# Optimization experiments

Measured on AMD Instinct MI355X. Metric: run time of the kernel, lower is better.

## Reference

```python
import jax, jax.numpy as jnp
import numpy as np

N, E, EV, D = 50000, 300000, 100000, 256
BN_EPS = 1e-5


def batchnorm(h, gamma, beta):
    # training-mode BN with batch statistics (biased var, matching torch normalization)
    mu = h.mean(axis=0)
    var = h.var(axis=0)
    return gamma * (h - mu) * jax.lax.rsqrt(var + BN_EPS) + beta


def mlp(h, W1, b1, g1, bt1, W2, b2):
    # Linear -> BN -> ReLU -> (Dropout=identity in eval) -> Linear
    h = h @ W1 + b1
    h = jax.nn.relu(batchnorm(h, g1, bt1))
    return h @ W2 + b2


def gine_conv(x, ei, ea, eps, W1, b1, g1, bt1, W2, b2):
    # message: ReLU(x_src + edge_attr); aggregate: scatter-add at dst; update: MLP((1+eps)*x + aggr)
    m = jax.nn.relu(x[ei[0]] + ea)                       # [E, D]
    aggr = jax.ops.segment_sum(m, ei[1], num_segments=N)  # [N, D]
    return mlp((1.0 + eps) * x + aggr, W1, b1, g1, bt1, W2, b2)


def setup_inputs() -> dict:
    key = jax.random.key(0)
    ks = jax.random.split(key, 16)
    s = 1.0 / np.sqrt(D)
    inp = {
        "x": jax.random.normal(ks[0], (N, D), jnp.float32),
        "edge_index": jax.random.randint(ks[1], (2, E), 0, N, jnp.int64),
        "edge_attr_emb": jax.random.normal(ks[2], (E, D), jnp.float32),
        "v_idx": jax.random.randint(ks[3], (2, EV), 0, N, jnp.int64),
        "v_edge_emb": jax.random.normal(ks[4], (EV, D), jnp.float32),
        # conv_down params
        "eps_down": jnp.zeros((), jnp.float32),
        "W1d": jax.random.normal(ks[5], (D, D), jnp.float32) * s,
        "b1d": jnp.zeros((D,), jnp.float32),
        "g1d": jnp.ones((D,), jnp.float32),
        "bt1d": jnp.zeros((D,), jnp.float32),
        "W2d": jax.random.normal(ks[6], (D, D), jnp.float32) * s,
        "b2d": jnp.zeros((D,), jnp.float32),
        # conv_up params
        "eps_up": jnp.zeros((), jnp.float32),
        "W1u": jax.random.normal(ks[7], (D, D), jnp.float32) * s,
        "b1u": jnp.zeros((D,), jnp.float32),
        "g1u": jnp.ones((D,), jnp.float32),
        "bt1u": jnp.zeros((D,), jnp.float32),
        "W2u": jax.random.normal(ks[8], (D, D), jnp.float32) * s,
        "b2u": jnp.zeros((D,), jnp.float32),
        # final BN + residual scales
        "bn_g": jnp.ones((D,), jnp.float32),
        "bn_b": jnp.zeros((D,), jnp.float32),
        "alpha1": jnp.asarray(1.0, jnp.float32),
        "alpha2": jnp.asarray(0.01, jnp.float32),
    }
    return inp


def reference(x, edge_index, edge_attr_emb, v_idx, v_edge_emb,
              eps_down, W1d, b1d, g1d, bt1d, W2d, b2d,
              eps_up, W1u, b1u, g1u, bt1u, W2u, b2u,
              bn_g, bn_b, alpha1, alpha2):
    h_down = gine_conv(x, edge_index, edge_attr_emb, eps_down, W1d, b1d, g1d, bt1d, W2d, b2d)
    h_up = gine_conv(x, v_idx, v_edge_emb, eps_up, W1u, b1u, g1u, bt1u, W2u, b2u)
    out = x + alpha1 * h_down + alpha2 * h_up
    return jax.nn.relu(batchnorm(out, bn_g, bn_b))
```

## Files before the change

### kernel.cpp

```cpp
#include <hip/hip_runtime.h>
#include <math.h>

#define N_NODES 50000
#define DIM 256
#define NE 300000
#define NEV 100000
#define BM 64
#define BK 64
#define NSLOT 8
#define GRID_PER ((N_NODES + BM - 1) / BM)

typedef float f32x4 __attribute__((ext_vector_type(4)));
typedef short s16x8 __attribute__((ext_vector_type(8)));

__device__ inline unsigned short f2bf(float f) {
    unsigned u = __float_as_uint(f);
    u += 0x7FFF + ((u >> 16) & 1);
    return (unsigned short)(u >> 16);
}
__device__ inline float bf2f(unsigned short s) {
    return __uint_as_float(((unsigned)s) << 16);
}
__device__ inline int swz(int row, int kg) {
    return row * BK + ((kg ^ (row & 7)) << 3);
}

__global__ __launch_bounds__(256) void prepw_kernel(
    const float* __restrict__ W1d, const float* __restrict__ W2d,
    const float* __restrict__ W1u, const float* __restrict__ W2u,
    unsigned short* __restrict__ Wt)
{
    int b = blockIdx.x;
    int w = b >> 8, n = b & 255, k = threadIdx.x;
    const float* W = (w == 0) ? W1d : (w == 1) ? W2d : (w == 2) ? W1u : W2u;
    Wt[(size_t)w * DIM * DIM + (size_t)n * DIM + k] = f2bf(W[(size_t)k * DIM + n]);
}

__global__ __launch_bounds__(256) void hist2_kernel(
    const int* __restrict__ ei, const int* __restrict__ vi,
    int* __restrict__ degD, int* __restrict__ degU)
{
    int i = blockIdx.x * blockDim.x + threadIdx.x;
    if (i < NE) atomicAdd(&degD[ei[NE + i]], 1);
    else if (i < NE + NEV) { int j = i - NE; atomicAdd(&degU[vi[NEV + j]], 1); }
}

__global__ __launch_bounds__(1024) void scan2_kernel(
    int* __restrict__ offD, int* __restrict__ curD,
    int* __restrict__ offU, int* __restrict__ curU)
{
    int* deg_offsets = (blockIdx.x == 0) ? offD : offU;
    int* cursor      = (blockIdx.x == 0) ? curD : curU;
    int E            = (blockIdx.x == 0) ? NE : NEV;
    __shared__ int part[1024];
    int t = threadIdx.x;
    const int CH = (N_NODES + 1023) / 1024;
    int beg = t * CH;
    int end = min(beg + CH, N_NODES);
    int s = 0;
    for (int i = beg; i < end; i++) s += deg_offsets[i];
    part[t] = s;
    __syncthreads();
    for (int off = 1; off < 1024; off <<= 1) {
        int v = part[t];
        int u = (t >= off) ? part[t - off] : 0;
        __syncthreads();
        part[t] = v + u;
        __syncthreads();
    }
    int run = (t > 0) ? part[t - 1] : 0;
    for (int i = beg; i < end; i++) {
        int dv = deg_offsets[i];
        deg_offsets[i] = run;
        cursor[i] = run;
        run += dv;
    }
    if (t == 1023) deg_offsets[N_NODES] = E;
}

__global__ __launch_bounds__(256) void fill2_kernel(
    const int* __restrict__ ei, const int* __restrict__ vi,
    int* __restrict__ curD, int* __restrict__ curU,
    int2* __restrict__ pairsD, int2* __restrict__ pairsU)
{
    int i = blockIdx.x * blockDim.x + threadIdx.x;
    if (i < NE) {
        int s = ei[i], d = ei[NE + i];
        int pos = atomicAdd(&curD[d], 1);
        pairsD[pos] = make_int2(i, s);
    } else if (i < NE + NEV) {
        int j = i - NE;
        int s = vi[j], d = vi[NEV + j];
        int pos = atomicAdd(&curU[d], 1);
        pairsU[pos] = make_int2(j, s);
    }
}

__device__ inline f32x4 ld4(const float* p) { return *(const f32x4*)p; }
__device__ inline f32x4 ldnt4(const float* p) {
    return __builtin_nontemporal_load((const f32x4*)p);
}
__device__ inline void acc_relu(f32x4& acc, f32x4 a, f32x4 b) {
    acc.x += fmaxf(a.x + b.x, 0.f);
    acc.y += fmaxf(a.y + b.y, 0.f);
    acc.z += fmaxf(a.z + b.z, 0.f);
    acc.w += fmaxf(a.w + b.w, 0.f);
}

__global__ __launch_bounds__(256) void gather2_kernel(
    const float* __restrict__ x, const float* __restrict__ ea,
    const float* __restrict__ vea,
    const int* __restrict__ offD, const int2* __restrict__ pairsD,
    const int* __restrict__ offU, const int2* __restrict__ pairsU,
    const float* __restrict__ epsd, const float* __restrict__ epsu,
    unsigned short* __restrict__ hD, unsigned short* __restrict__ hU)
{
    __shared__ f32x4 part[2][64];
    int warp = threadIdx.x >> 6;
    int lane = threadIdx.x & 63;
    int slotn = warp >> 1;
    int half = warp & 1;
    int nidx = blockIdx.x * 2 + slotn;
    bool down = nidx < N_NODES;
    int node = down ? nidx : nidx - N_NODES;
    const int* off      = down ? offD   : offU;
    const int2* pairs   = down ? pairsD : pairsU;
    const float* eat    = down ? ea     : vea;
    unsigned short* h   = down ? hD     : hU;
    float epsv = 1.0f + (down ? epsd[0] : epsu[0]);

    int beg = off[node], end = off[node + 1];
    f32x4 acc = {0.f, 0.f, 0.f, 0.f};
    int cofs = lane * 4;
    int p = beg + half;
    for (; p + 2 < end; p += 4) {
        int2 q0 = pairs[p], q1 = pairs[p + 2];
        f32x4 a0 = ld4(x + (size_t)q0.y * DIM + cofs);
        f32x4 b0 = ldnt4(eat + (size_t)q0.x * DIM + cofs);
        f32x4 a1 = ld4(x + (size_t)q1.y * DIM + cofs);
        f32x4 b1 = ldnt4(eat + (size_t)q1.x * DIM + cofs);
        acc_relu(acc, a0, b0);
        acc_relu(acc, a1, b1);
    }
    if (p < end) {
        int2 q0 = pairs[p];
        f32x4 a0 = ld4(x + (size_t)q0.y * DIM + cofs);
        f32x4 b0 = ldnt4(eat + (size_t)q0.x * DIM + cofs);
        acc_relu(acc, a0, b0);
    }
    if (half == 1) part[slotn][lane] = acc;
    __syncthreads();
    if (half == 0) {
        f32x4 o = part[slotn][lane];
        acc.x += o.x; acc.y += o.y; acc.z += o.z; acc.w += o.w;
        f32x4 xv = ld4(x + (size_t)node * DIM + cofs);
        acc.x = fmaf(epsv, xv.x, acc.x);
        acc.y = fmaf(epsv, xv.y, acc.y);
        acc.z = fmaf(epsv, xv.z, acc.z);
        acc.w = fmaf(epsv, xv.w, acc.w);
        ushort4 pk;
        pk.x = f2bf(acc.x); pk.y = f2bf(acc.y);
        pk.z = f2bf(acc.z); pk.w = f2bf(acc.w);
        *(ushort4*)(h + (size_t)node * DIM + cofs) = pk;
    }
}

__global__ __launch_bounds__(256) void scatter_kernel(
    const float* __restrict__ x, const float* __restrict__ ea,
    const int* __restrict__ idx, int E, float* __restrict__ buf)
{
    int wid = blockIdx.x * (blockDim.x >> 6) + (threadIdx.x >> 6);
    int lane = threadIdx.x & 63;
    if (wid >= E) return;
    int s = idx[wid];
    int d = idx[E + wid];
    float4 a = ((const float4*)(x + (size_t)s * DIM))[lane];
    float4 b = ((const float4*)(ea + (size_t)wid * DIM))[lane];
    float* dst = buf + (size_t)d * DIM + lane * 4;
    atomicAdd(dst + 0, fmaxf(a.x + b.x, 0.f));
    atomicAdd(dst + 1, fmaxf(a.y + b.y, 0.f));
    atomicAdd(dst + 2, fmaxf(a.z + b.z, 0.f));
    atomicAdd(dst + 3, fmaxf(a.w + b.w, 0.f));
}

__global__ __launch_bounds__(256) void conv_kernel(
    const float* __restrict__ x, const float* __restrict__ aggr,
    const float* __restrict__ eps_p, unsigned short* __restrict__ h)
{
    float epsv = 1.0f + eps_p[0];
    int i = blockIdx.x * blockDim.x + threadIdx.x;
    const int total = N_NODES * (DIM / 4);
    for (int f = i; f < total; f += gridDim.x * blockDim.x) {
        float4 xv = ((const float4*)x)[f];
        float4 av = ((const float4*)aggr)[f];
        ushort4 pk;
        pk.x = f2bf(fmaf(epsv, xv.x, av.x));
        pk.y = f2bf(fmaf(epsv, xv.y, av.y));
        pk.z = f2bf(fmaf(epsv, xv.z, av.z));
        pk.w = f2bf(fmaf(epsv, xv.w, av.w));
        ((ushort4*)h)[f] = pk;
    }
}

__global__ __launch_bounds__(256) void gemm1_both(
    const unsigned short* __restrict__ hD, const unsigned short* __restrict__ hU,
    const unsigned short* __restrict__ Wt1d, const unsigned short* __restrict__ Wt1u,
    const float* __restrict__ b1d, const float* __restrict__ b1u,
    unsigned short* __restrict__ t1D, unsigned short* __restrict__ t1U,
    float* __restrict__ sumD, float* __restrict__ sqD,
    float* __restrict__ sumU, float* __restrict__ sqU)
{
    __shared__ unsigned short As[BM * BK];
    __shared__ unsigned short Bs[DIM * BK];
    int blk = blockIdx.x;
    bool down = blk < GRID_PER;
    int bb = down ? blk : blk - GRID_PER;
    const unsigned short* h  = down ? hD   : hU;
    const unsigned short* Wt = down ? Wt1d : Wt1u;
    const float* bias        = down ? b1d  : b1u;
    unsigned short* t1       = down ? t1D  : t1U;
    float* ssum              = down ? sumD : sumU;
    float* ssq               = down ? sqD  : sqU;

    int t = threadIdx.x;
    int w = t >> 6, l = t & 63, lrow = l & 15, kgrp = l >> 4;
    int row0 = bb * BM;

    f32x4 acc[16];
    #pragma unroll
    for (int i = 0; i < 16; ++i) acc[i] = (f32x4){0.f, 0.f, 0.f, 0.f};

    for (int k0 = 0; k0 < DIM; k0 += BK) {
        __syncthreads();
        #pragma unroll
        for (int it = 0; it < 2; ++it) {
            int g = it * 256 + t, row = g >> 3, kg = g & 7;
            int gr = row0 + row;
            s16x8 v = {0, 0, 0, 0, 0, 0, 0, 0};
            if (gr < N_NODES)
                v = *(const s16x8*)&h[(size_t)gr * DIM + k0 + kg * 8];
            *(s16x8*)&As[swz(row, kg)] = v;
        }
        #pragma unroll
        for (int it = 0; it < 8; ++it) {
            int g = it * 256 + t, row = g >> 3, kg = g & 7;
            s16x8 v = *(const s16x8*)&Wt[(size_t)row * DIM + k0 + kg * 8];
            *(s16x8*)&Bs[swz(row, kg)] = v;
        }
        __syncthreads();
        #pragma unroll
        for (int kk = 0; kk < 2; ++kk) {
            s16x8 af[4], bf[4];
            #pragma unroll
            for (int mi = 0; mi < 4; ++mi)
                af[mi] = *(const s16x8*)&As[swz(mi * 16 + lrow, kk * 4 + kgrp)];
            #pragma unroll
            for (int ni = 0; ni < 4; ++ni)
                bf[ni] = *(const s16x8*)&Bs[swz(w * 64 + ni * 16 + lrow, kk * 4 + kgrp)];
            #pragma unroll
            for (int mi = 0; mi < 4; ++mi)
                #pragma unroll
                for (int ni = 0; ni < 4; ++ni)
                    acc[mi * 4 + ni] = __builtin_amdgcn_mfma_f32_16x16x32_bf16(
                        af[mi], bf[ni], acc[mi * 4 + ni], 0, 0, 0);
        }
    }
    int slot = bb & (NSLOT - 1);
    #pragma unroll
    for (int ni = 0; ni < 4; ++ni) {
        int col = w * 64 + ni * 16 + lrow;
        float bv = bias[col];
        float s = 0.f, q = 0.f;
        #pragma unroll
        for (int mi = 0; mi < 4; ++mi) {
            #pragma unroll
            for (int r = 0; r < 4; ++r) {
                int grow = row0 + mi * 16 + kgrp * 4 + r;
                if (grow < N_NODES) {
                    float v = acc[mi * 4 + ni][r] + bv;
                    t1[(size_t)grow * DIM + col] = f2bf(v);
                    s += v; q += v * v;
                }
            }
        }
        s += __shfl_xor(s, 16); q += __shfl_xor(q, 16);
        s += __shfl_xor(s, 32); q += __shfl_xor(q, 32);
        if (kgrp == 0) {
            atomicAdd(&ssum[slot * DIM + col], s);
            atomicAdd(&ssq[slot * DIM + col], q);
        }
    }
}

__device__ inline void bn_finalize(
    const float* ssum, const float* ssq, const float* g, const float* b,
    float* scale, float* shift, int c)
{
    float s = 0.f, q = 0.f;
    #pragma unroll
    for (int k = 0; k < NSLOT; ++k) { s += ssum[k * DIM + c]; q += ssq[k * DIM + c]; }
    const float invN = 1.0f / (float)N_NODES;
    float mu = s * invN;
    float var = q * invN - mu * mu;
    float sc = g[c] * rsqrtf(var + 1e-5f);
    scale[c] = sc;
    shift[c] = b[c] - mu * sc;
}

__global__ __launch_bounds__(256) void gemm2_fused(
    const unsigned short* __restrict__ t1D, const unsigned short* __restrict__ t1U,
    const float* __restrict__ sumD, const float* __restrict__ sqD,
    const float* __restrict__ g1d, const float* __restrict__ bt1d,
    const float* __restrict__ sumU, const float* __restrict__ sqU,
    const float* __restrict__ g1u, const float* __restrict__ bt1u,
    const unsigned short* __restrict__ Wt2d, const unsigned short* __restrict__ Wt2u,
    const float* __restrict__ b2d, const float* __restrict__ b2u,
    const float* __restrict__ a1, const float* __restrict__ a2,
    const float* __restrict__ x, float* __restrict__ out,
    float* __restrict__ sumF, float* __restrict__ sqF)
{
    __shared__ unsigned short As[BM * BK];
    __shared__ unsigned short Bs[DIM * BK];
    __shared__ float scDl[DIM], shDl[DIM], scUl[DIM], shUl[DIM];
    int t = threadIdx.x;
    int w = t >> 6, l = t & 63, lrow = l & 15, kgrp = l >> 4;
    int bb = blockIdx.x;
    int row0 = bb * BM;

    bn_finalize(sumD, sqD, g1d, bt1d, scDl, shDl, t);
    bn_finalize(sumU, sqU, g1u, bt1u, scUl, shUl, t);
    float a1v = a1[0], a2v = a2[0];

    f32x4 acc[16], accO[16];
    #pragma unroll
    for (int i = 0; i < 16; ++i) acc[i] = (f32x4){0.f, 0.f, 0.f, 0.f};

    for (int k0 = 0; k0 < DIM; k0 += BK) {
        __syncthreads();
        #pragma unroll
        for (int it = 0; it < 2; ++it) {
            int g = it * 256 + t, row = g >> 3, kg = g & 7;
            int gr = row0 + row;
            s16x8 pack = {0, 0, 0, 0, 0, 0, 0, 0};
            if (gr < N_NODES) {
                s16x8 tv = *(const s16x8*)(t1D + (size_t)gr * DIM + k0 + kg * 8);
                #pragma unroll
                for (int j = 0; j < 8; ++j) {
                    int c = k0 + kg * 8 + j;
                    pack[j] = f2bf(fmaxf(fmaf(bf2f((unsigned short)tv[j]), scDl[c], shDl[c]), 0.f));
                }
            }
            *(s16x8*)&As[swz(row, kg)] = pack;
        }
        #pragma unroll
        for (int it = 0; it < 8; ++it) {
            int g = it * 256 + t, row = g >> 3, kg = g & 7;
            s16x8 v = *(const s16x8*)&Wt2d[(size_t)row * DIM + k0 + kg * 8];
            *(s16x8*)&Bs[swz(row, kg)] = v;
        }
        __syncthreads();
        #pragma unroll
        for (int kk = 0; kk < 2; ++kk) {
            s16x8 af[4], bf[4];
            #pragma unroll
            for (int mi = 0; mi < 4; ++mi)
                af[mi] = *(const s16x8*)&As[swz(mi * 16 + lrow, kk * 4 + kgrp)];
            #pragma unroll
            for (int ni = 0; ni < 4; ++ni)
                bf[ni] = *(const s16x8*)&Bs[swz(w * 64 + ni * 16 + lrow, kk * 4 + kgrp)];
            #pragma unroll
            for (int mi = 0; mi < 4; ++mi)
                #pragma unroll
                for (int ni = 0; ni < 4; ++ni)
                    acc[mi * 4 + ni] = __builtin_amdgcn_mfma_f32_16x16x32_bf16(
                        af[mi], bf[ni], acc[mi * 4 + ni], 0, 0, 0);
        }
    }
    #pragma unroll
    for (int ni = 0; ni < 4; ++ni) {
        float bv = b2d[w * 64 + ni * 16 + lrow];
        #pragma unroll
        for (int mi = 0; mi < 4; ++mi) {
            #pragma unroll
            for (int r = 0; r < 4; ++r)
                accO[mi * 4 + ni][r] = a1v * (acc[mi * 4 + ni][r] + bv);
            acc[mi * 4 + ni] = (f32x4){0.f, 0.f, 0.f, 0.f};
        }
    }

    for (int k0 = 0; k0 < DIM; k0 += BK) {
        __syncthreads();
        #pragma unroll
        for (int it = 0; it < 2; ++it) {
            int g = it * 256 + t, row = g >> 3, kg = g & 7;
            int gr = row0 + row;
            s16x8 pack = {0, 0, 0, 0, 0, 0, 0, 0};
            if (gr < N_NODES) {
                s16x8 tv = *(const s16x8*)(t1U + (size_t)gr * DIM + k0 + kg * 8);
                #pragma unroll
                for (int j = 0; j < 8; ++j) {
                    int c = k0 + kg * 8 + j;
                    pack[j] = f2bf(fmaxf(fmaf(bf2f((unsigned short)tv[j]), scUl[c], shUl[c]), 0.f));
                }
            }
            *(s16x8*)&As[swz(row, kg)] = pack;
        }
        #pragma unroll
        for (int it = 0; it < 8; ++it) {
            int g = it * 256 + t, row = g >> 3, kg = g & 7;
            s16x8 v = *(const s16x8*)&Wt2u[(size_t)row * DIM + k0 + kg * 8];
            *(s16x8*)&Bs[swz(row, kg)] = v;
        }
        __syncthreads();
        #pragma unroll
        for (int kk = 0; kk < 2; ++kk) {
            s16x8 af[4], bf[4];
            #pragma unroll
            for (int mi = 0; mi < 4; ++mi)
                af[mi] = *(const s16x8*)&As[swz(mi * 16 + lrow, kk * 4 + kgrp)];
            #pragma unroll
            for (int ni = 0; ni < 4; ++ni)
                bf[ni] = *(const s16x8*)&Bs[swz(w * 64 + ni * 16 + lrow, kk * 4 + kgrp)];
            #pragma unroll
            for (int mi = 0; mi < 4; ++mi)
                #pragma unroll
                for (int ni = 0; ni < 4; ++ni)
                    acc[mi * 4 + ni] = __builtin_amdgcn_mfma_f32_16x16x32_bf16(
                        af[mi], bf[ni], acc[mi * 4 + ni], 0, 0, 0);
        }
    }

    int slot = bb & (NSLOT - 1);
    #pragma unroll
    for (int ni = 0; ni < 4; ++ni) {
        int col = w * 64 + ni * 16 + lrow;
        float bvU = b2u[col];
        float s = 0.f, q = 0.f;
        #pragma unroll
        for (int mi = 0; mi < 4; ++mi) {
            #pragma unroll
            for (int r = 0; r < 4; ++r) {
                int grow = row0 + mi * 16 + kgrp * 4 + r;
                if (grow < N_NODES) {
                    size_t o = (size_t)grow * DIM + col;
                    float v = x[o] + accO[mi * 4 + ni][r]
                            + a2v * (acc[mi * 4 + ni][r] + bvU);
                    out[o] = v;
                    s += v; q += v * v;
                }
            }
        }
        s += __shfl_xor(s, 16); q += __shfl_xor(q, 16);
        s += __shfl_xor(s, 32); q += __shfl_xor(q, 32);
        if (kgrp == 0) {
            atomicAdd(&sumF[slot * DIM + col], s);
            atomicAdd(&sqF[slot * DIM + col], q);
        }
    }
}

__global__ __launch_bounds__(256) void bnrelu_kernel(
    float* __restrict__ out,
    const float* __restrict__ sumF, const float* __restrict__ sqF,
    const float* __restrict__ bng, const float* __restrict__ bnb)
{
    __shared__ float scl[DIM], shl[DIM];
    bn_finalize(sumF, sqF, bng, bnb, scl, shl, threadIdx.x);
    __syncthreads();
    int idx = blockIdx.x * blockDim.x + threadIdx.x;
    const int total = N_NODES * (DIM / 4);
    for (int f = idx; f < total; f += gridDim.x * blockDim.x) {
        float4 v = ((float4*)out)[f];
        int c = (f * 4) & (DIM - 1);
        float4 sc = *(const float4*)(scl + c);
        float4 sh = *(const float4*)(shl + c);
        v.x = fmaxf(v.x * sc.x + sh.x, 0.0f);
        v.y = fmaxf(v.y * sc.y + sh.y, 0.0f);
        v.z = fmaxf(v.z * sc.z + sh.z, 0.0f);
        v.w = fmaxf(v.w * sc.w + sh.w, 0.0f);
        ((float4*)out)[f] = v;
    }
}

extern "C" void kernel_launch(void* const* d_in, const int* in_sizes, int n_in,
                              void* d_out, int out_size, void* d_ws, size_t ws_size,
                              hipStream_t stream)
{
    const float* x    = (const float*)d_in[0];
    const int*   ei   = (const int*)  d_in[1];
    const float* ea   = (const float*)d_in[2];
    const int*   vi   = (const int*)  d_in[3];
    const float* vea  = (const float*)d_in[4];
    const float* epsd = (const float*)d_in[5];
    const float* W1d  = (const float*)d_in[6];
    const float* b1d  = (const float*)d_in[7];
    const float* g1d  = (const float*)d_in[8];
    const float* bt1d = (const float*)d_in[9];
    const float* W2d  = (const float*)d_in[10];
    const float* b2d  = (const float*)d_in[11];
    const float* epsu = (const float*)d_in[12];
    const float* W1u  = (const float*)d_in[13];
    const float* b1u  = (const float*)d_in[14];
    const float* g1u  = (const float*)d_in[15];
    const float* bt1u = (const float*)d_in[16];
    const float* W2u  = (const float*)d_in[17];
    const float* b2u  = (const float*)d_in[18];
    const float* bng  = (const float*)d_in[19];
    const float* bnb  = (const float*)d_in[20];
    const float* a1   = (const float*)d_in[21];
    const float* a2   = (const float*)d_in[22];

    float* out = (float*)d_out;

    char* p = (char*)d_ws;
    unsigned short* hD  = (unsigned short*)p;  p += (size_t)N_NODES * DIM * 2;
    unsigned short* hU  = (unsigned short*)p;  p += (size_t)N_NODES * DIM * 2;
    unsigned short* t1D = (unsigned short*)p;  p += (size_t)N_NODES * DIM * 2;
    unsigned short* t1U = (unsigned short*)p;  p += (size_t)N_NODES * DIM * 2;
    unsigned short* Wt  = (unsigned short*)p;  p += (size_t)4 * DIM * DIM * 2;
    char* zero_base = p;
    float* stats = (float*)p;                  p += (size_t)6 * NSLOT * DIM * 4;
    int* offD = (int*)p;                       p += (size_t)(N_NODES + 1) * 4;
    int* offU = (int*)p;                       p += (size_t)(N_NODES + 1) * 4;
    size_t zero_bytes = (size_t)(p - zero_base);
    int* curD = (int*)p;                       p += (size_t)N_NODES * 4;
    int* curU = (int*)p;                       p += (size_t)N_NODES * 4;
    char* union_base = p;
    int2* pairsD = (int2*)p;                   p += (size_t)NE * 8;
    int2* pairsU = (int2*)p;                   p += (size_t)NEV * 8;
    size_t need_csr = (size_t)(p - (char*)d_ws);
    float* aggr = (float*)union_base;
    size_t need_fb = (size_t)(union_base - (char*)d_ws) + (size_t)N_NODES * DIM * 4;
    bool use_csr = ws_size >= need_csr;

    float* sumD = stats;
    float* sqD  = stats + 1 * NSLOT * DIM;
    float* sumU = stats + 2 * NSLOT * DIM;
    float* sqU  = stats + 3 * NSLOT * DIM;
    float* sumF = stats + 4 * NSLOT * DIM;
    float* sqF  = stats + 5 * NSLOT * DIM;

    unsigned short* Wt1d = Wt;
    unsigned short* Wt2d = Wt + 1 * (size_t)DIM * DIM;
    unsigned short* Wt1u = Wt + 2 * (size_t)DIM * DIM;
    unsigned short* Wt2u = Wt + 3 * (size_t)DIM * DIM;

    hipMemsetAsync(zero_base, 0, zero_bytes, stream);
    prepw_kernel<<<4 * DIM, 256, 0, stream>>>(W1d, W2d, W1u, W2u, Wt);

    if (use_csr) {
        hist2_kernel<<<(NE + NEV + 255) / 256, 256, 0, stream>>>(ei, vi, offD, offU);
        scan2_kernel<<<2, 1024, 0, stream>>>(offD, curD, offU, curU);
        fill2_kernel<<<(NE + NEV + 255) / 256, 256, 0, stream>>>(
            ei, vi, curD, curU, pairsD, pairsU);
        gather2_kernel<<<N_NODES, 256, 0, stream>>>(
            x, ea, vea, offD, pairsD, offU, pairsU, epsd, epsu, hD, hU);
    } else if (ws_size >= need_fb) {
        hipMemsetAsync(aggr, 0, (size_t)N_NODES * DIM * 4, stream);
        scatter_kernel<<<(NE + 3) / 4, 256, 0, stream>>>(x, ea, ei, NE, aggr);
        conv_kernel<<<2048, 256, 0, stream>>>(x, aggr, epsd, hD);
        hipMemsetAsync(aggr, 0, (size_t)N_NODES * DIM * 4, stream);
        scatter_kernel<<<(NEV + 3) / 4, 256, 0, stream>>>(x, vea, vi, NEV, aggr);
        conv_kernel<<<2048, 256, 0, stream>>>(x, aggr, epsu, hU);
    }

    gemm1_both<<<2 * GRID_PER, 256, 0, stream>>>(
        hD, hU, Wt1d, Wt1u, b1d, b1u, t1D, t1U, sumD, sqD, sumU, sqU);

    gemm2_fused<<<GRID_PER, 256, 0, stream>>>(
        t1D, t1U, sumD, sqD, g1d, bt1d, sumU, sqU, g1u, bt1u,
        Wt2d, Wt2u, b2d, b2u, a1, a2, x, out, sumF, sqF);

    bnrelu_kernel<<<2048, 256, 0, stream>>>(out, sumF, sqF, bng, bnb);
}
```

Before: 438.4 us.

## Gather from bf16 x copy, pre-swizzle operands, use global_load_lds in GEMMs

Result: faster. 415.1 us (-5.3%).

```diff
diff --git a/kernel.cpp b/kernel.cpp
--- a/kernel.cpp
+++ b/kernel.cpp
@@ -9,6 +9,9 @@
 #define BK 64
 #define NSLOT 8
 #define GRID_PER ((N_NODES + BM - 1) / BM)
+#define PREP_W_BLOCKS (4 * DIM)
+#define PREP_X_BLOCKS 1024
+#define HIST_BLOCKS ((NE + NEV + 255) / 256)
 
 typedef float f32x4 __attribute__((ext_vector_type(4)));
 typedef short s16x8 __attribute__((ext_vector_type(8)));
@@ -24,25 +27,51 @@
 __device__ inline int swz(int row, int kg) {
     return row * BK + ((kg ^ (row & 7)) << 3);
 }
-
-__global__ __launch_bounds__(256) void prepw_kernel(
+__device__ inline void gl16(const unsigned short* g, unsigned short* l) {
+    __builtin_amdgcn_global_load_lds(
+        (const __attribute__((address_space(1))) void*)g,
+        (__attribute__((address_space(3))) void*)l, 16, 0, 0);
+}
+__device__ inline int hdst(int node, int lane) {
+    return ((lane >> 4) << 6) + (((((lane >> 1) & 7)) ^ (node & 7)) << 3)
+         + ((lane & 1) << 2);
+}
+
+__global__ __launch_bounds__(256) void prep_kernel(
     const float* __restrict__ W1d, const float* __restrict__ W2d,
     const float* __restrict__ W1u, const float* __restrict__ W2u,
-    unsigned short* __restrict__ Wt)
-{
-    int b = blockIdx.x;
-    int w = b >> 8, n = b & 255, k = threadIdx.x;
-    const float* W = (w == 0) ? W1d : (w == 1) ? W2d : (w == 2) ? W1u : W2u;
-    Wt[(size_t)w * DIM * DIM + (size_t)n * DIM + k] = f2bf(W[(size_t)k * DIM + n]);
-}
-
-__global__ __launch_bounds__(256) void hist2_kernel(
+    unsigned short* __restrict__ Wt,
+    const float* __restrict__ x, unsigned short* __restrict__ xb,
     const int* __restrict__ ei, const int* __restrict__ vi,
     int* __restrict__ degD, int* __restrict__ degU)
 {
-    int i = blockIdx.x * blockDim.x + threadIdx.x;
-    if (i < NE) atomicAdd(&degD[ei[NE + i]], 1);
-    else if (i < NE + NEV) { int j = i - NE; atomicAdd(&degU[vi[NEV + j]], 1); }
+    int b = blockIdx.x, t = threadIdx.x;
+    if (b < PREP_W_BLOCKS) {
+        int w = b >> 8, n = b & 255;
+        const float* W = (w == 0) ? W1d : (w == 1) ? W2d : (w == 2) ? W1u : W2u;
+        int k0 = (t >> 6) << 6, kg = (t >> 3) & 7, j = t & 7;
+        int src = k0 + ((kg ^ (n & 7)) << 3) + j;
+        Wt[(size_t)w * DIM * DIM + (size_t)n * DIM + t] =
+            f2bf(W[(size_t)src * DIM + n]);
+    } else if (b < PREP_W_BLOCKS + PREP_X_BLOCKS) {
+        int idx = (b - PREP_W_BLOCKS) * 256 + t;
+        const int stride = PREP_X_BLOCKS * 256;
+        const int total = N_NODES * (DIM / 8);
+        for (int f = idx; f < total; f += stride) {
+            float4 v0 = ((const float4*)x)[f * 2];
+            float4 v1 = ((const float4*)x)[f * 2 + 1];
+            s16x8 pk;
+            pk[0] = f2bf(v0.x); pk[1] = f2bf(v0.y);
+            pk[2] = f2bf(v0.z); pk[3] = f2bf(v0.w);
+            pk[4] = f2bf(v1.x); pk[5] = f2bf(v1.y);
+            pk[6] = f2bf(v1.z); pk[7] = f2bf(v1.w);
+            *(s16x8*)(xb + (size_t)f * 8) = pk;
+        }
+    } else {
+        int i = (b - PREP_W_BLOCKS - PREP_X_BLOCKS) * 256 + t;
+        if (i < NE) atomicAdd(&degD[ei[NE + i]], 1);
+        else if (i < NE + NEV) { int j2 = i - NE; atomicAdd(&degU[vi[NEV + j2]], 1); }
+    }
 }
 
 __global__ __launch_bounds__(1024) void scan2_kernel(
@@ -96,9 +125,13 @@
     }
 }
 
-__device__ inline f32x4 ld4(const float* p) { return *(const f32x4*)p; }
 __device__ inline f32x4 ldnt4(const float* p) {
     return __builtin_nontemporal_load((const f32x4*)p);
+}
+__device__ inline f32x4 bf4f(ushort4 v) {
+    f32x4 r;
+    r.x = bf2f(v.x); r.y = bf2f(v.y); r.z = bf2f(v.z); r.w = bf2f(v.w);
+    return r;
 }
 __device__ inline void acc_relu(f32x4& acc, f32x4 a, f32x4 b) {
     acc.x += fmaxf(a.x + b.x, 0.f);
@@ -108,7 +141,7 @@
 }
 
 __global__ __launch_bounds__(256) void gather2_kernel(
-    const float* __restrict__ x, const float* __restrict__ ea,
+    const unsigned short* __restrict__ xb, const float* __restrict__ ea,
     const float* __restrict__ vea,
     const int* __restrict__ offD, const int2* __restrict__ pairsD,
     const int* __restrict__ offU, const int2* __restrict__ pairsU,
@@ -135,25 +168,25 @@
     int p = beg + half;
     for (; p + 2 < end; p += 4) {
         int2 q0 = pairs[p], q1 = pairs[p + 2];
-        f32x4 a0 = ld4(x + (size_t)q0.y * DIM + cofs);
+        ushort4 a0 = *(const ushort4*)(xb + (size_t)q0.y * DIM + cofs);
         f32x4 b0 = ldnt4(eat + (size_t)q0.x * DIM + cofs);
-        f32x4 a1 = ld4(x + (size_t)q1.y * DIM + cofs);
+        ushort4 a1 = *(const ushort4*)(xb + (size_t)q1.y * DIM + cofs);
         f32x4 b1 = ldnt4(eat + (size_t)q1.x * DIM + cofs);
-        acc_relu(acc, a0, b0);
-        acc_relu(acc, a1, b1);
+        acc_relu(acc, bf4f(a0), b0);
+        acc_relu(acc, bf4f(a1), b1);
     }
     if (p < end) {
         int2 q0 = pairs[p];
-        f32x4 a0 = ld4(x + (size_t)q0.y * DIM + cofs);
+        ushort4 a0 = *(const ushort4*)(xb + (size_t)q0.y * DIM + cofs);
         f32x4 b0 = ldnt4(eat + (size_t)q0.x * DIM + cofs);
-        acc_relu(acc, a0, b0);
+        acc_relu(acc, bf4f(a0), b0);
     }
     if (half == 1) part[slotn][lane] = acc;
     __syncthreads();
     if (half == 0) {
         f32x4 o = part[slotn][lane];
         acc.x += o.x; acc.y += o.y; acc.z += o.z; acc.w += o.w;
-        f32x4 xv = ld4(x + (size_t)node * DIM + cofs);
+        f32x4 xv = bf4f(*(const ushort4*)(xb + (size_t)node * DIM + cofs));
         acc.x = fmaf(epsv, xv.x, acc.x);
         acc.y = fmaf(epsv, xv.y, acc.y);
         acc.z = fmaf(epsv, xv.z, acc.z);
@@ -161,7 +194,7 @@
         ushort4 pk;
         pk.x = f2bf(acc.x); pk.y = f2bf(acc.y);
         pk.z = f2bf(acc.z); pk.w = f2bf(acc.w);
-        *(ushort4*)(h + (size_t)node * DIM + cofs) = pk;
+        *(ushort4*)(h + (size_t)node * DIM + hdst(node, lane)) = pk;
     }
 }
 
@@ -189,16 +222,18 @@
 {
     float epsv = 1.0f + eps_p[0];
     int i = blockIdx.x * blockDim.x + threadIdx.x;
-    const int total = N_NODES * (DIM / 4);
+    const int total = N_NODES * 64;
     for (int f = i; f < total; f += gridDim.x * blockDim.x) {
-        float4 xv = ((const float4*)x)[f];
-        float4 av = ((const float4*)aggr)[f];
+        int node = f >> 6, lane = f & 63;
+        size_t o = (size_t)node * DIM + lane * 4;
+        float4 xv = *(const float4*)(x + o);
+        float4 av = *(const float4*)(aggr + o);
         ushort4 pk;
         pk.x = f2bf(fmaf(epsv, xv.x, av.x));
         pk.y = f2bf(fmaf(epsv, xv.y, av.y));
         pk.z = f2bf(fmaf(epsv, xv.z, av.z));
         pk.w = f2bf(fmaf(epsv, xv.w, av.w));
-        ((ushort4*)h)[f] = pk;
+        *(ushort4*)(h + (size_t)node * DIM + hdst(node, lane)) = pk;
     }
 }
 
@@ -234,18 +269,15 @@
         __syncthreads();
         #pragma unroll
         for (int it = 0; it < 2; ++it) {
-            int g = it * 256 + t, row = g >> 3, kg = g & 7;
-            int gr = row0 + row;
-            s16x8 v = {0, 0, 0, 0, 0, 0, 0, 0};
-            if (gr < N_NODES)
-                v = *(const s16x8*)&h[(size_t)gr * DIM + k0 + kg * 8];
-            *(s16x8*)&As[swz(row, kg)] = v;
+            int g = it * 256 + t;
+            gl16(h + (size_t)(row0 + (g >> 3)) * DIM + k0 + ((g & 7) << 3),
+                 &As[g << 3]);
         }
         #pragma unroll
         for (int it = 0; it < 8; ++it) {
-            int g = it * 256 + t, row = g >> 3, kg = g & 7;
-            s16x8 v = *(const s16x8*)&Wt[(size_t)row * DIM + k0 + kg * 8];
-            *(s16x8*)&Bs[swz(row, kg)] = v;
+            int g = it * 256 + t;
+            gl16(Wt + (size_t)(g >> 3) * DIM + k0 + ((g & 7) << 3),
+                 &Bs[g << 3]);
         }
         __syncthreads();
         #pragma unroll
@@ -335,98 +367,65 @@
     #pragma unroll
     for (int i = 0; i < 16; ++i) acc[i] = (f32x4){0.f, 0.f, 0.f, 0.f};
 
-    for (int k0 = 0; k0 < DIM; k0 += BK) {
-        __syncthreads();
-        #pragma unroll
-        for (int it = 0; it < 2; ++it) {
-            int g = it * 256 + t, row = g >> 3, kg = g & 7;
-            int gr = row0 + row;
-            s16x8 pack = {0, 0, 0, 0, 0, 0, 0, 0};
-            if (gr < N_NODES) {
-                s16x8 tv = *(const s16x8*)(t1D + (size_t)gr * DIM + k0 + kg * 8);
+    #pragma unroll
+    for (int phase = 0; phase < 2; ++phase) {
+        const unsigned short* t1 = phase == 0 ? t1D : t1U;
+        const unsigned short* Wt = phase == 0 ? Wt2d : Wt2u;
+        const float* scl = phase == 0 ? scDl : scUl;
+        const float* shl = phase == 0 ? shDl : shUl;
+        for (int k0 = 0; k0 < DIM; k0 += BK) {
+            __syncthreads();
+            #pragma unroll
+            for (int it = 0; it < 8; ++it) {
+                int g = it * 256 + t;
+                gl16(Wt + (size_t)(g >> 3) * DIM + k0 + ((g & 7) << 3),
+                     &Bs[g << 3]);
+            }
+            #pragma unroll
+            for (int it = 0; it < 2; ++it) {
+                int g = it * 256 + t, row = g >> 3, kg = g & 7;
+                int gr = row0 + row;
+                s16x8 pack = {0, 0, 0, 0, 0, 0, 0, 0};
+                if (gr < N_NODES) {
+                    s16x8 tv = *(const s16x8*)(t1 + (size_t)gr * DIM + k0 + kg * 8);
+                    #pragma unroll
+                    for (int j = 0; j < 8; ++j) {
+                        int c = k0 + kg * 8 + j;
+                        pack[j] = f2bf(fmaxf(fmaf(bf2f((unsigned short)tv[j]), scl[c], shl[c]), 0.f));
+                    }
+                }
+                *(s16x8*)&As[swz(row, kg)] = pack;
+            }
+            __syncthreads();
+            #pragma unroll
+            for (int kk = 0; kk < 2; ++kk) {
+                s16x8 af[4], bf[4];
                 #pragma unroll
-                for (int j = 0; j < 8; ++j) {
-                    int c = k0 + kg * 8 + j;
-                    pack[j] = f2bf(fmaxf(fmaf(bf2f((unsigned short)tv[j]), scDl[c], shDl[c]), 0.f));
+                for (int mi = 0; mi < 4; ++mi)
+                    af[mi] = *(const s16x8*)&As[swz(mi * 16 + lrow, kk * 4 + kgrp)];
+                #pragma unroll
+                for (int ni = 0; ni < 4; ++ni)
+                    bf[ni] = *(const s16x8*)&Bs[swz(w * 64 + ni * 16 + lrow, kk * 4 + kgrp)];
+                #pragma unroll
+                for (int mi = 0; mi < 4; ++mi)
+                    #pragma unroll
+                    for (int ni = 0; ni < 4; ++ni)
+                        acc[mi * 4 + ni] = __builtin_amdgcn_mfma_f32_16x16x32_bf16(
+                            af[mi], bf[ni], acc[mi * 4 + ni], 0, 0, 0);
+            }
+        }
+        if (phase == 0) {
+            #pragma unroll
+            for (int ni = 0; ni < 4; ++ni) {
+                float bv = b2d[w * 64 + ni * 16 + lrow];
+                #pragma unroll
+                for (int mi = 0; mi < 4; ++mi) {
+                    #pragma unroll
+                    for (int r = 0; r < 4; ++r)
+                        accO[mi * 4 + ni][r] = a1v * (acc[mi * 4 + ni][r] + bv);
+                    acc[mi * 4 + ni] = (f32x4){0.f, 0.f, 0.f, 0.f};
                 }
             }
-            *(s16x8*)&As[swz(row, kg)] = pack;
-        }
-        #pragma unroll
-        for (int it = 0; it < 8; ++it) {
-            int g = it * 256 + t, row = g >> 3, kg = g & 7;
-            s16x8 v = *(const s16x8*)&Wt2d[(size_t)row * DIM + k0 + kg * 8];
-            *(s16x8*)&Bs[swz(row, kg)] = v;
-        }
-        __syncthreads();
-        #pragma unroll
-        for (int kk = 0; kk < 2; ++kk) {
-            s16x8 af[4], bf[4];
-            #pragma unroll
-            for (int mi = 0; mi < 4; ++mi)
-                af[mi] = *(const s16x8*)&As[swz(mi * 16 + lrow, kk * 4 + kgrp)];
-            #pragma unroll
-            for (int ni = 0; ni < 4; ++ni)
-                bf[ni] = *(const s16x8*)&Bs[swz(w * 64 + ni * 16 + lrow, kk * 4 + kgrp)];
-            #pragma unroll
-            for (int mi = 0; mi < 4; ++mi)
-                #pragma unroll
-                for (int ni = 0; ni < 4; ++ni)
-                    acc[mi * 4 + ni] = __builtin_amdgcn_mfma_f32_16x16x32_bf16(
-                        af[mi], bf[ni], acc[mi * 4 + ni], 0, 0, 0);
-        }
-    }
-    #pragma unroll
-    for (int ni = 0; ni < 4; ++ni) {
-        float bv = b2d[w * 64 + ni * 16 + lrow];
-        #pragma unroll
-        for (int mi = 0; mi < 4; ++mi) {
-            #pragma unroll
-            for (int r = 0; r < 4; ++r)
-                accO[mi * 4 + ni][r] = a1v * (acc[mi * 4 + ni][r] + bv);
-            acc[mi * 4 + ni] = (f32x4){0.f, 0.f, 0.f, 0.f};
-        }
-    }
-
-    for (int k0 = 0; k0 < DIM; k0 += BK) {
-        __syncthreads();
-        #pragma unroll
-        for (int it = 0; it < 2; ++it) {
-            int g = it * 256 + t, row = g >> 3, kg = g & 7;
-            int gr = row0 + row;
-            s16x8 pack = {0, 0, 0, 0, 0, 0, 0, 0};
-            if (gr < N_NODES) {
-                s16x8 tv = *(const s16x8*)(t1U + (size_t)gr * DIM + k0 + kg * 8);
-                #pragma unroll
-                for (int j = 0; j < 8; ++j) {
-                    int c = k0 + kg * 8 + j;
-                    pack[j] = f2bf(fmaxf(fmaf(bf2f((unsigned short)tv[j]), scUl[c], shUl[c]), 0.f));
-                }
-            }
-            *(s16x8*)&As[swz(row, kg)] = pack;
-        }
-        #pragma unroll
-        for (int it = 0; it < 8; ++it) {
-            int g = it * 256 + t, row = g >> 3, kg = g & 7;
-            s16x8 v = *(const s16x8*)&Wt2u[(size_t)row * DIM + k0 + kg * 8];
-            *(s16x8*)&Bs[swz(row, kg)] = v;
-        }
-        __syncthreads();
-        #pragma unroll
-        for (int kk = 0; kk < 2; ++kk) {
-            s16x8 af[4], bf[4];
-            #pragma unroll
-            for (int mi = 0; mi < 4; ++mi)
-                af[mi] = *(const s16x8*)&As[swz(mi * 16 + lrow, kk * 4 + kgrp)];
-            #pragma unroll
-            for (int ni = 0; ni < 4; ++ni)
-                bf[ni] = *(const s16x8*)&Bs[swz(w * 64 + ni * 16 + lrow, kk * 4 + kgrp)];
-            #pragma unroll
-            for (int mi = 0; mi < 4; ++mi)
-                #pragma unroll
-                for (int ni = 0; ni < 4; ++ni)
-                    acc[mi * 4 + ni] = __builtin_amdgcn_mfma_f32_16x16x32_bf16(
-                        af[mi], bf[ni], acc[mi * 4 + ni], 0, 0, 0);
         }
     }
 
@@ -517,6 +516,7 @@
     unsigned short* hU  = (unsigned short*)p;  p += (size_t)N_NODES * DIM * 2;
     unsigned short* t1D = (unsigned short*)p;  p += (size_t)N_NODES * DIM * 2;
     unsigned short* t1U = (unsigned short*)p;  p += (size_t)N_NODES * DIM * 2;
+    unsigned short* xb  = (unsigned short*)p;  p += (size_t)N_NODES * DIM * 2;
     unsigned short* Wt  = (unsigned short*)p;  p += (size_t)4 * DIM * DIM * 2;
     char* zero_base = p;
     float* stats = (float*)p;                  p += (size_t)6 * NSLOT * DIM * 4;
@@ -546,16 +546,18 @@
     unsigned short* Wt2u = Wt + 3 * (size_t)DIM * DIM;
 
     hipMemsetAsync(zero_base, 0, zero_bytes, stream);
-    prepw_kernel<<<4 * DIM, 256, 0, stream>>>(W1d, W2d, W1u, W2u, Wt);
 
     if (use_csr) {
-        hist2_kernel<<<(NE + NEV + 255) / 256, 256, 0, stream>>>(ei, vi, offD, offU);
+        prep_kernel<<<PREP_W_BLOCKS + PREP_X_BLOCKS + HIST_BLOCKS, 256, 0, stream>>>(
+            W1d, W2d, W1u, W2u, Wt, x, xb, ei, vi, offD, offU);
         scan2_kernel<<<2, 1024, 0, stream>>>(offD, curD, offU, curU);
         fill2_kernel<<<(NE + NEV + 255) / 256, 256, 0, stream>>>(
             ei, vi, curD, curU, pairsD, pairsU);
         gather2_kernel<<<N_NODES, 256, 0, stream>>>(
-            x, ea, vea, offD, pairsD, offU, pairsU, epsd, epsu, hD, hU);
+            xb, ea, vea, offD, pairsD, offU, pairsU, epsd, epsu, hD, hU);
     } else if (ws_size >= need_fb) {
+        prep_kernel<<<PREP_W_BLOCKS + PREP_X_BLOCKS, 256, 0, stream>>>(
+            W1d, W2d, W1u, W2u, Wt, x, xb, ei, vi, offD, offU);
         hipMemsetAsync(aggr, 0, (size_t)N_NODES * DIM * 4, stream);
         scatter_kernel<<<(NE + 3) / 4, 256, 0, stream>>>(x, ea, ei, NE, aggr);
         conv_kernel<<<2048, 256, 0, stream>>>(x, aggr, epsd, hD);
```
